# Performance work log

Hardware: AMD Instinct MI355X
Metric: run time of the kernel (lower is better)

Reference implementation:

```python
import jax, jax.numpy as jnp
import numpy as np

WEIGHT = 0.1

SOBEL_X = jnp.array([[-1.,0.,1.],[-2.,0.,2.],[-1.,0.,1.]], jnp.float32).reshape(1,1,3,3)
SOBEL_Y = jnp.array([[-1.,-2.,-1.],[0.,0.,0.],[1.,2.,1.]], jnp.float32).reshape(1,1,3,3)
LAPLACIAN = jnp.array([[0.,1.,0.],[1.,-4.,1.],[0.,1.,0.]], jnp.float32).reshape(1,1,3,3)


def _conv3x3(x, k):
    # x: [B,1,H,W], k: [1,1,3,3], SAME padding (pad=1)
    return jax.lax.conv_general_dilated(x, k, (1, 1), ((1, 1), (1, 1)),
                                         dimension_numbers=('NCHW', 'OIHW', 'NCHW'))


def _extract_dem_features(dem):
    gx = _conv3x3(dem, SOBEL_X)
    gy = _conv3x3(dem, SOBEL_Y)
    gmag = jnp.sqrt(gx * gx + gy * gy + 1e-8)
    gmag = (gmag - gmag.min()) / (gmag.max() - gmag.min() + 1e-8)  # global min/max like torch
    hnorm = (dem - dem.min()) / (dem.max() - dem.min() + 1e-8)
    curv = jnp.tanh(_conv3x3(dem, LAPLACIAN) * 0.1)
    return jnp.concatenate([gmag, hnorm, curv], axis=1)  # [B,3,H,W]


def _connectivity_one(mask):
    # mask: [H,W] float32 in {0,1}; 4-connected component labeling via min-label propagation
    H, W = mask.shape
    sentinel = H * W
    fg = mask > 0
    init = jnp.where(fg, jnp.arange(H * W, dtype=jnp.int32).reshape(H, W), sentinel)

    def body(state):
        lbl, _ = state
        pad = jnp.pad(lbl, 1, constant_values=sentinel)
        nb = jnp.minimum(jnp.minimum(pad[:-2, 1:-1], pad[2:, 1:-1]),
                         jnp.minimum(pad[1:-1, :-2], pad[1:-1, 2:]))
        new = jnp.where(fg, jnp.minimum(lbl, nb), sentinel)
        return new, jnp.any(new != lbl)

    lbl, _ = jax.lax.while_loop(lambda s: s[1], body, (init, jnp.array(True)))
    sizes = jax.ops.segment_sum(mask.reshape(-1), lbl.reshape(-1), num_segments=sentinel + 1)[:sentinel]
    total = mask.sum()
    ratio = sizes.max() / jnp.maximum(total, 1.0)
    # matches scipy path: 0 if no components; (1 - main_region_ratio) otherwise
    # (single component gives ratio==1 -> 0, same as scipy's len(sizes)>1 branch)
    return jnp.where(total > 0, 1.0 - ratio, 0.0)


def _connectivity_loss(pred_prob):
    mask = (pred_prob[:, 0] > 0.5).astype(jnp.float32)  # [B,H,W]
    per_sample = jax.vmap(_connectivity_one)(mask)
    return per_sample.sum() / pred_prob.shape[0]


def _scale_consistency_loss(pred_prob):
    B, _, H, W = pred_prob.shape
    area = pred_prob.sum(axis=(1, 2, 3))
    total_pixels = H * W
    tmin, tmax = 0.1 * total_pixels, 0.3 * total_pixels
    loss = jnp.mean(jax.nn.relu(area - tmax) + jax.nn.relu(tmin - area))
    return loss / total_pixels


def reference(pred_prob, dem):
    dem_features = _extract_dem_features(dem)              # [B,3,H,W]
    pred_features = jnp.broadcast_to(pred_prob, dem_features.shape)
    similarity = jnp.mean((pred_features - dem_features) ** 2)
    conn = _connectivity_loss(pred_prob)
    scale = _scale_consistency_loss(pred_prob)
    total = similarity + 0.1 * conn + 0.05 * scale
    return WEIGHT * total


def setup_inputs() -> dict:
    key = jax.random.key(0)
    k1, k2 = jax.random.split(key)
    B, H, W = 16, 512, 512
    pred_prob = jax.random.uniform(k1, (B, 1, H, W), dtype=jnp.float32)  # post-sigmoid probs
    dem = jax.random.normal(k2, (B, 1, H, W), dtype=jnp.float32)
    return {"pred_prob": pred_prob, "dem": dem}
```

## Files before the change

### kernel.cpp

```cpp
#include <hip/hip_runtime.h>
#include <math.h>

#define IMG_B 16
#define IMG_H 512
#define IMG_W 512
#define IMG_HW (IMG_H * IMG_W)
#define NPART 2048

#define NMOM 9

#define TILES 256
#define NODES_PER_TILE 192
#define NODES_PER_IMG (TILES * NODES_PER_TILE)
#define PAIRS 128
#define TOUCH (1 << 30)

struct Scal {
    float gmin, gmax, dmin, dmax;
    double mom[NMOM];
    double area[IMG_B];
    int fgcnt[IMG_B];
    int maxcnt[IMG_B];
};

#define OFF_PMM   512
#define OFF_MOM   33280
#define OFF_FG    180736
#define OFF_SCR   188928

__device__ __forceinline__ int uf_findv(const int* L, int p) {
    while (true) { const int q = ((volatile const int*)L)[p]; if (q == p) return p; p = q; }
}
__device__ __forceinline__ void uf_merge(int* L, int a, int b) {
    while (true) {
        a = uf_findv(L, a);
        b = uf_findv(L, b);
        if (a == b) return;
        if (a < b) { int t = a; a = b; b = t; }
        const int old = atomicMin(&L[a], b);
        if (old == a) return;
        a = old;
    }
}

__device__ __forceinline__ int run_start(unsigned m, int b) {
    const unsigned below = ~m & ((b == 0) ? 0u : ((1u << b) - 1u));
    return below ? (int)(32u - (unsigned)__builtin_clz(below)) : 0;
}
__device__ __forceinline__ int run_len(unsigned m, int s) {
    const unsigned inv = ~(m >> s);
    return inv ? __builtin_ctz(inv) : (32 - s);
}
__device__ __forceinline__ int run_idx(unsigned sm, int c) {
    return __popc(sm & (unsigned)((2ull << c) - 1ull)) - 1;
}
__device__ __forceinline__ unsigned spread4(unsigned x) {
    x &= 0xFFu;
    x = (x | (x << 12)) & 0x000F000Fu;
    x = (x | (x << 6))  & 0x03030303u;
    x = (x | (x << 3))  & 0x11111111u;
    return x;
}

__device__ __forceinline__ void ring_decode(int i, int& x, int& y) {
    if (i < 32)      { x = i;      y = 0;      }
    else if (i < 64) { x = i - 32; y = 31;     }
    else if (i < 94) { x = 0;      y = i - 63; }
    else             { x = 31;     y = i - 93; }
}

__global__ void k_main(const float* __restrict__ dem, const float* __restrict__ pred,
                       float4* __restrict__ pmm, double* __restrict__ pblk,
                       int* __restrict__ pfg,
                       int* __restrict__ Lp, int* __restrict__ Cp,
                       int* __restrict__ nslot, int* __restrict__ pairmax,
                       int b0, int nloc, int featOn) {
    __shared__ double smem_d[4104];
    int* smem = (int*)smem_d;
    const int tid = threadIdx.x;
    const int lane = tid & 63, wid = tid >> 6;

    if (blockIdx.x >= 32) {
        if (!featOn) return;
        const int fb = blockIdx.x - 32;
        const int b = blockIdx.y;
        const size_t off = (size_t)b * IMG_HW;
        const float* d = dem + off;
        const float* p = pred + off;
        const int base = fb * 2048 + tid * 8;
        const int y = base >> 9;

        const float4 z4 = make_float4(0.f, 0.f, 0.f, 0.f);
        float4 m0 = *(const float4*)(d + base);
        float4 m1 = *(const float4*)(d + base + 4);
        float4 u0 = z4, u1 = z4, w0 = z4, w1 = z4;
        if (y > 0)   { u0 = *(const float4*)(d + base - 512); u1 = *(const float4*)(d + base - 508); }
        if (y < 511) { w0 = *(const float4*)(d + base + 512); w1 = *(const float4*)(d + base + 516); }

        float uu[10], mm[10], ww[10];
        { float t;
          t = __shfl(m1.w, lane - 1); mm[0] = (lane > 0)  ? t : 0.f;
          t = __shfl(m0.x, lane + 1); mm[9] = (lane < 63) ? t : 0.f;
          t = __shfl(u1.w, lane - 1); uu[0] = (lane > 0)  ? t : 0.f;
          t = __shfl(u0.x, lane + 1); uu[9] = (lane < 63) ? t : 0.f;
          t = __shfl(w1.w, lane - 1); ww[0] = (lane > 0)  ? t : 0.f;
          t = __shfl(w0.x, lane + 1); ww[9] = (lane < 63) ? t : 0.f; }
        uu[1]=u0.x; uu[2]=u0.y; uu[3]=u0.z; uu[4]=u0.w; uu[5]=u1.x; uu[6]=u1.y; uu[7]=u1.z; uu[8]=u1.w;
        mm[1]=m0.x; mm[2]=m0.y; mm[3]=m0.z; mm[4]=m0.w; mm[5]=m1.x; mm[6]=m1.y; mm[7]=m1.z; mm[8]=m1.w;
        ww[1]=w0.x; ww[2]=w0.y; ww[3]=w0.z; ww[4]=w0.w; ww[5]=w1.x; ww[6]=w1.y; ww[7]=w1.z; ww[8]=w1.w;

        const float4 p0 = *(const float4*)(p + base);
        const float4 p1 = *(const float4*)(p + base + 4);
        const float pv[8] = {p0.x, p0.y, p0.z, p0.w, p1.x, p1.y, p1.z, p1.w};

        float gmn = 3.4e38f, gmx = -3.4e38f, dmn = 3.4e38f, dmx = -3.4e38f;
        float mf[NMOM];
#pragma unroll
        for (int m = 0; m < NMOM; ++m) mf[m] = 0.f;
        int fg = 0;
#pragma unroll
        for (int j = 0; j < 8; ++j) {
            const float gx = (uu[j+2] - uu[j]) + 2.f * (mm[j+2] - mm[j]) + (ww[j+2] - ww[j]);
            const float gy = (ww[j] - uu[j]) + 2.f * (ww[j+1] - uu[j+1]) + (ww[j+2] - uu[j+2]);
            const float gm = sqrtf(gx * gx + gy * gy + 1e-8f);
            const float lap = uu[j+1] + mm[j] + mm[j+2] + ww[j+1] - 4.f * mm[j+1];
            const float cv = tanhf(lap * 0.1f);
            const float pj = pv[j], dj = mm[j+1];
            gmn = fminf(gmn, gm); gmx = fmaxf(gmx, gm);
            dmn = fminf(dmn, dj); dmx = fmaxf(dmx, dj);
            fg += (pj > 0.5f) ? 1 : 0;
            const float et = pj - cv;
            mf[0] += pj;  mf[1] += pj * pj;
            mf[2] += gm;  mf[3] += gm * gm;  mf[4] += pj * gm;
            mf[5] += dj;  mf[6] += dj * dj;  mf[7] += pj * dj;
            mf[8] += et * et;
        }

        for (int o = 32; o > 0; o >>= 1) {
            gmn = fminf(gmn, __shfl_down(gmn, o));
            gmx = fmaxf(gmx, __shfl_down(gmx, o));
            dmn = fminf(dmn, __shfl_down(dmn, o));
            dmx = fmaxf(dmx, __shfl_down(dmx, o));
#pragma unroll
            for (int m = 0; m < NMOM; ++m) mf[m] += __shfl_down(mf[m], o);
            fg += __shfl_down(fg, o);
        }
        double (*sa)[NMOM] = (double(*)[NMOM])smem_d;
        float* sg0 = (float*)(smem_d + 36);
        float* sg1 = sg0 + 4; float* sd0 = sg0 + 8; float* sd1 = sg0 + 12;
        int* sf = (int*)(sg0 + 16);
        if (lane == 0) {
            sg0[wid] = gmn; sg1[wid] = gmx; sd0[wid] = dmn; sd1[wid] = dmx; sf[wid] = fg;
#pragma unroll
            for (int m = 0; m < NMOM; ++m) sa[wid][m] = (double)mf[m];
        }
        __syncthreads();
        if (tid == 0) {
            double mo[NMOM];
#pragma unroll
            for (int m = 0; m < NMOM; ++m) mo[m] = sa[0][m];
            for (int w = 1; w < 4; ++w) {
                gmn = fminf(gmn, sg0[w]); gmx = fmaxf(gmx, sg1[w]);
                dmn = fminf(dmn, sd0[w]); dmx = fmaxf(dmx, sd1[w]);
                fg += sf[w];
#pragma unroll
                for (int m = 0; m < NMOM; ++m) mo[m] += sa[w][m];
            }
            const int bid = b * 128 + fb;
            pmm[bid] = make_float4(gmn, gmx, dmn, dmx);
#pragma unroll
            for (int m = 0; m < NMOM; ++m) pblk[(size_t)bid * NMOM + m] = mo[m];
            pfg[bid] = fg;
        }
        return;
    }

    if (blockIdx.y >= nloc) return;
    const int slot = blockIdx.y;
    const float* p = pred + (size_t)(b0 + slot) * IMG_HW;
    int* L = Lp + (size_t)slot * NODES_PER_IMG;
    int* C = Cp + (size_t)slot * NODES_PER_IMG;
    const int pair = blockIdx.x * 4 + wid;
    const int tile0 = pair * 2;
    const int half = lane >> 5;
    const int tile = tile0 + half;
    const int tx0 = (tile0 & 15) * 32;
    const int ty  = (tile0 >> 4) * 32;
    const int r = lane & 31;

    int* lab  = smem;
    int* lcnt = smem + 4096;
    int* ns   = smem + 8192;
    int* labw = lab + wid * 1024;
    int* lcw  = lcnt + wid * 1024;
    int* nsw  = ns + wid * 2;
    if (lane < 2) nsw[lane] = 0;
    const int nbase = half * 512;

    const int myit = r >> 2;
    unsigned long long q0 = 0, q1 = 0, q2 = 0, q3 = 0;
    for (int it = 0; it < 8; ++it) {
        const int row = it * 4 + (lane >> 4);
        const float4 v = *(const float4*)(p + (ty + row) * IMG_W + tx0 + (lane & 15) * 4);
        const unsigned long long t0 = __ballot(v.x > 0.5f);
        const unsigned long long t1 = __ballot(v.y > 0.5f);
        const unsigned long long t2 = __ballot(v.z > 0.5f);
        const unsigned long long t3 = __ballot(v.w > 0.5f);
        if (it == myit) { q0 = t0; q1 = t1; q2 = t2; q3 = t3; }
    }
#pragma unroll
    for (int k = 0; k < 16; ++k) {
        const int n = k * 64 + lane;
        labw[n] = n; lcw[n] = 0;
    }
    const int sh = 16 * (r & 3) + 8 * half;
    const unsigned m = spread4((unsigned)(q0 >> sh))
                     | (spread4((unsigned)(q1 >> sh)) << 1)
                     | (spread4((unsigned)(q2 >> sh)) << 2)
                     | (spread4((unsigned)(q3 >> sh)) << 3);
    const int mpl = __shfl((int)m, lane - 1);
    const unsigned mp = (r >= 1) ? (unsigned)mpl : 0u;

    const unsigned sm  = m  & ~(m << 1);
    const unsigned smp = mp & ~(mp << 1);

    if (r >= 1) {
        unsigned ov = m & mp;
        while (ov) {
            const int bpos = __builtin_ctz(ov);
            const int sa2 = run_start(m, bpos);
            const int ea = sa2 + run_len(m, sa2) - 1;
            const int sb = run_start(mp, bpos);
            const int eb = sb + run_len(mp, sb) - 1;
            uf_merge(labw, nbase + run_idx(sm, sa2) * 32 + r,
                            nbase + run_idx(smp, sb) * 32 + (r - 1));
            const int e = (ea < eb) ? ea : eb;
            ov = (e >= 31) ? 0u : (ov & ~((1u << (e + 1)) - 1u));
        }
    }

    {
        unsigned rs = sm; int j = 0;
        while (rs) {
            const int st = __builtin_ctz(rs); rs &= rs - 1;
            const int len = run_len(m, st);
            const int e = st + len - 1;
            const int node = nbase + j * 32 + r; ++j;
            const int root = uf_findv(labw, node);
            if (root != node) labw[node] = root;
            atomicAdd(&lcw[root], len);
            if (r == 0 || r == 31 || st == 0 || e == 31)
                atomicOr(&lcw[root], TOUCH);
        }
    }

    int locmax = 0;
    {
        unsigned rs = sm; int j = 0;
        while (rs) {
            rs &= rs - 1;
            const int node = nbase + j * 32 + r; ++j;
            if (labw[node] != node) continue;
            const int c = lcw[node];
            if (c & TOUCH) {
                const int sl = atomicAdd(&nsw[half], 1);
                const int gn = tile * NODES_PER_TILE + 128 + sl;
                L[gn] = gn;
                C[gn] = c & ~TOUCH;
                lcw[node] = gn;
            } else {
                locmax = max(locmax, c);
            }
        }
    }
    for (int o = 32; o > 0; o >>= 1) locmax = max(locmax, __shfl_down(locmax, o));

#pragma unroll
    for (int t = 0; t < 4; ++t) {
        const int i = lane + t * 64;
        const int h = i >> 7, idx = i & 127;
        const int tb = (tile0 + h) * NODES_PER_TILE;
        if (idx < 124) {
            int x, yy;
            ring_decode(idx, x, yy);
            const unsigned my = (unsigned)__shfl((int)m, h * 32 + yy);
            int val = -1;
            if ((my >> x) & 1u) {
                const unsigned smy = my & ~(my << 1);
                const int node = h * 512 + run_idx(smy, x) * 32 + yy;
                const int root = uf_findv(labw, node);
                val = lcw[root];
            }
            L[tb + idx] = val;
        } else {
            L[tb + idx] = -1;
        }
    }

    if (lane == 0) pairmax[slot * PAIRS + pair] = locmax;
    if (lane < 2) nslot[slot * TILES + tile0 + lane] = nsw[lane];
}

__global__ void k_red(const float4* __restrict__ pmm, const double* __restrict__ pblk,
                      const int* __restrict__ pfg, Scal* s) {
    const int wid = threadIdx.x >> 6, lane = threadIdx.x & 63;
    if (blockIdx.x < IMG_B) {
        const int b = blockIdx.x;
        double ar = 0.0; int fg = 0;
        if (threadIdx.x < 128) {
            const int k = b * 128 + threadIdx.x;
            ar = pblk[(size_t)k * NMOM + 0];
            fg = pfg[k];
        }
        for (int o = 32; o > 0; o >>= 1) { ar += __shfl_down(ar, o); fg += __shfl_down(fg, o); }
        __shared__ double sa[4];
        __shared__ int sf[4];
        if (lane == 0) { sa[wid] = ar; sf[wid] = fg; }
        __syncthreads();
        if (threadIdx.x == 0) {
            ar += sa[1]; fg += sf[1];
            s->area[b] = ar; s->fgcnt[b] = fg;
            s->maxcnt[b] = 0;
        }
    } else if (blockIdx.x == IMG_B) {
        float gmn = 3.4e38f, gmx = -3.4e38f, dmn = 3.4e38f, dmx = -3.4e38f;
        for (int k = threadIdx.x; k < NPART; k += 256) {
            const float4 v = pmm[k];
            gmn = fminf(gmn, v.x); gmx = fmaxf(gmx, v.y);
            dmn = fminf(dmn, v.z); dmx = fmaxf(dmx, v.w);
        }
        for (int o = 32; o > 0; o >>= 1) {
            gmn = fminf(gmn, __shfl_down(gmn, o));
            gmx = fmaxf(gmx, __shfl_down(gmx, o));
            dmn = fminf(dmn, __shfl_down(dmn, o));
            dmx = fmaxf(dmx, __shfl_down(dmx, o));
        }
        __shared__ float sg0[4], sg1[4], sd0[4], sd1[4];
        if (lane == 0) { sg0[wid] = gmn; sg1[wid] = gmx; sd0[wid] = dmn; sd1[wid] = dmx; }
        __syncthreads();
        if (threadIdx.x == 0) {
            for (int w = 1; w < 4; ++w) {
                gmn = fminf(gmn, sg0[w]); gmx = fmaxf(gmx, sg1[w]);
                dmn = fminf(dmn, sd0[w]); dmx = fmaxf(dmx, sd1[w]);
            }
            s->gmin = gmn; s->gmax = gmx; s->dmin = dmn; s->dmax = dmx;
        }
    } else {
        const int m = blockIdx.x - IMG_B - 1;
        double acc = 0.0;
        for (int k = threadIdx.x; k < NPART; k += 256) acc += pblk[(size_t)k * NMOM + m];
        for (int o = 32; o > 0; o >>= 1) acc += __shfl_down(acc, o);
        __shared__ double sa[4];
        if (lane == 0) sa[wid] = acc;
        __syncthreads();
        if (threadIdx.x == 0) {
            for (int w = 1; w < 4; ++w) acc += sa[w];
            s->mom[m] = acc;
        }
    }
}

__global__ void k_bmerge(int* __restrict__ Lp) {
    const int slot = blockIdx.y;
    int* L = Lp + (size_t)slot * NODES_PER_IMG;
    const int e = blockIdx.x * 256 + threadIdx.x;
    int a, b;
    if (e < 7680) {
        const int sc = e / 512, y = e - sc * 512;
        const int ly = y & 31;
        const int tL = (y >> 5) * 16 + sc;
        const int iL = (ly == 0) ? 31 : (ly == 31) ? 63 : (93 + ly);
        const int iR = (ly == 0) ? 0  : (ly == 31) ? 32 : (63 + ly);
        a = tL * NODES_PER_TILE + iL;
        b = (tL + 1) * NODES_PER_TILE + iR;
    } else {
        const int e2 = e - 7680;
        const int sr = e2 / 512, x = e2 - sr * 512;
        const int lx = x & 31;
        const int tT = sr * 16 + (x >> 5);
        a = tT * NODES_PER_TILE + 32 + lx;
        b = (tT + 16) * NODES_PER_TILE + lx;
    }
    if (L[a] >= 0 && L[b] >= 0) uf_merge(L, a, b);
}

__global__ void k_lflush(const int* __restrict__ Lp, int* __restrict__ Cp,
                         const int* __restrict__ nslot) {
    const int img = blockIdx.y;
    const int* L = Lp + (size_t)img * NODES_PER_IMG;
    int* C = Cp + (size_t)img * NODES_PER_IMG;
    const int sidx = blockIdx.x * 256 + threadIdx.x;
    const int tile = sidx >> 6, sl = sidx & 63;
    if (sl >= nslot[img * TILES + tile]) return;
    const int g = tile * NODES_PER_TILE + 128 + sl;
    const int rt = uf_findv(L, g);
    if (rt != g) atomicAdd(&C[rt], C[g]);
}

__global__ void k_lmax(const int* __restrict__ Lp, const int* __restrict__ Cp,
                       const int* __restrict__ nslot, const int* __restrict__ pairmax,
                       Scal* s, int b0) {
    const int img = blockIdx.y;
    int m = 0;
    if (blockIdx.x < 64) {
        const int* L = Lp + (size_t)img * NODES_PER_IMG;
        const int* C = Cp + (size_t)img * NODES_PER_IMG;
        const int sidx = blockIdx.x * 256 + threadIdx.x;
        const int tile = sidx >> 6, sl = sidx & 63;
        if (sl < nslot[img * TILES + tile]) {
            const int g = tile * NODES_PER_TILE + 128 + sl;
            if (L[g] == g) m = C[g];
        }
    } else {
        if (threadIdx.x < PAIRS) m = pairmax[img * PAIRS + threadIdx.x];
    }
    for (int o = 32; o > 0; o >>= 1) m = max(m, __shfl_down(m, o));
    __shared__ int sm[4];
    const int wid = threadIdx.x >> 6, lane = threadIdx.x & 63;
    if (lane == 0) sm[wid] = m;
    __syncthreads();
    if (threadIdx.x == 0) {
        for (int w = 1; w < 4; ++w) m = max(m, sm[w]);
        if (m > 0) atomicMax(&s->maxcnt[b0 + img], m);
    }
}

__global__ void k_final(const Scal* __restrict__ s, float* __restrict__ out) {
    const double N = (double)IMG_B * (double)IMG_HW;
    const float gdenf = s->gmax - s->gmin + 1e-8f;
    const float ddenf = s->dmax - s->dmin + 1e-8f;
    const double a = 1.0 / (double)gdenf, bb = 1.0 / (double)ddenf;
    const double gmin = (double)s->gmin, dmin = (double)s->dmin;
    const double S_p = s->mom[0], S_pp = s->mom[1];
    const double S_g = s->mom[2], S_gg = s->mom[3], S_pg = s->mom[4];
    const double S_d = s->mom[5], S_dd = s->mom[6], S_pd = s->mom[7];
    const double S_t = s->mom[8];
    const double sum_g = S_pp - 2.0 * a * (S_pg - gmin * S_p)
                       + a * a * (S_gg - 2.0 * gmin * S_g + gmin * gmin * N);
    const double sum_d = S_pp - 2.0 * bb * (S_pd - dmin * S_p)
                       + bb * bb * (S_dd - 2.0 * dmin * S_d + dmin * dmin * N);
    const double sim = (sum_g + sum_d + S_t) / (3.0 * N);

    const double tp = (double)IMG_HW;
    const double tmin = 0.1 * tp, tmax = 0.3 * tp;
    double conn = 0.0, scale = 0.0;
    for (int b = 0; b < IMG_B; ++b) {
        const int total = s->fgcnt[b];
        if (total > 0) conn += 1.0 - (double)s->maxcnt[b] / (double)total;
        const double ar = s->area[b];
        scale += fmax(ar - tmax, 0.0) + fmax(tmin - ar, 0.0);
    }
    conn /= (double)IMG_B;
    scale = (scale / (double)IMG_B) / tp;
    const double total = sim + 0.1 * conn + 0.05 * scale;
    out[0] = (float)(0.1 * total);
}

extern "C" void kernel_launch(void* const* d_in, const int* in_sizes, int n_in,
                              void* d_out, int out_size, void* d_ws, size_t ws_size,
                              hipStream_t stream) {
    const float* pred = (const float*)d_in[0];
    const float* dem  = (const float*)d_in[1];
    float* out = (float*)d_out;

    char* ws = (char*)d_ws;
    Scal* s = (Scal*)ws;
    float4* pmm  = (float4*)(ws + OFF_PMM);
    double* pblk = (double*)(ws + OFF_MOM);
    int*    pfg  = (int*)(ws + OFF_FG);
    int* scratch = (int*)(ws + OFF_SCR);
    const size_t avail_ints = (ws_size > OFF_SCR) ? (ws_size - OFF_SCR) / 4 : 0;
    const size_t per_img = 2ull * NODES_PER_IMG + TILES + PAIRS;

    long long chunk = (long long)(avail_ints / per_img);
    if (chunk < 1) chunk = 1;
    if (chunk > IMG_B) chunk = IMG_B;

    for (int b0 = 0; b0 < IMG_B; b0 += (int)chunk) {
        const int n = (int)((b0 + chunk <= IMG_B) ? chunk : (IMG_B - b0));
        int* Lp      = scratch;
        int* Cp      = scratch + (size_t)chunk * NODES_PER_IMG;
        int* nslotp  = scratch + 2ull * chunk * NODES_PER_IMG;
        int* pairmax = nslotp + (size_t)chunk * TILES;
        const int featOn = (b0 == 0) ? 1 : 0;
        const int gx = featOn ? 160 : 32;
        const int gy = featOn ? IMG_B : n;
        hipLaunchKernelGGL(k_main, dim3(gx, gy), dim3(256), 0, stream,
                           dem, pred, pmm, pblk, pfg, Lp, Cp, nslotp, pairmax,
                           b0, n, featOn);
        if (b0 == 0)
            hipLaunchKernelGGL(k_red, dim3(IMG_B + 1 + NMOM), dim3(256), 0, stream,
                               pmm, pblk, pfg, s);
        hipLaunchKernelGGL(k_bmerge, dim3(60, n), dim3(256), 0, stream, Lp);
        hipLaunchKernelGGL(k_lflush, dim3(64, n), dim3(256), 0, stream, Lp, Cp, nslotp);
        hipLaunchKernelGGL(k_lmax,   dim3(65, n), dim3(256), 0, stream,
                           Lp, Cp, nslotp, pairmax, s, b0);
    }

    hipLaunchKernelGGL(k_final, dim3(1), dim3(1), 0, stream, s, out);
}
```

Baseline: 69.07 us.

## Halve k_main block size and fuse label flush with max into one tail kernel

Drops k_main to 128 threads per block with twice as many blocks, so feature blocks cover 1024 pixels and CCL blocks hold two tile pairs, and partial buffers, offsets and the k_red reduction are resized to match. It also merges k_lflush and k_lmax into a single k_tail kernel. Each non-root boundary slot adds its count to its root and uses the atomicAdd return value as a candidate maximum, removing one launch and its grid-wide barrier. The running atomic sums should still reach the final component size at the last add, but this relies on the per-slot counts being final before the atomics run.

```diff
diff --git a/kernel.cpp b/kernel.cpp
--- a/kernel.cpp
+++ b/kernel.cpp
@@ -5,7 +5,7 @@
 #define IMG_H 512
 #define IMG_W 512
 #define IMG_HW (IMG_H * IMG_W)
-#define NPART 2048
+#define NPART 4096
 
 #define NMOM 9
 
@@ -24,9 +24,9 @@
 };
 
 #define OFF_PMM   512
-#define OFF_MOM   33280
-#define OFF_FG    180736
-#define OFF_SCR   188928
+#define OFF_MOM   66048
+#define OFF_FG    360960
+#define OFF_SCR   377344
 
 __device__ __forceinline__ int uf_findv(const int* L, int p) {
     while (true) { const int q = ((volatile const int*)L)[p]; if (q == p) return p; p = q; }
@@ -75,19 +75,19 @@
                        int* __restrict__ Lp, int* __restrict__ Cp,
                        int* __restrict__ nslot, int* __restrict__ pairmax,
                        int b0, int nloc, int featOn) {
-    __shared__ double smem_d[4104];
+    __shared__ double smem_d[2052];
     int* smem = (int*)smem_d;
     const int tid = threadIdx.x;
     const int lane = tid & 63, wid = tid >> 6;
 
-    if (blockIdx.x >= 32) {
+    if (blockIdx.x >= 64) {
         if (!featOn) return;
-        const int fb = blockIdx.x - 32;
+        const int fb = blockIdx.x - 64;
         const int b = blockIdx.y;
         const size_t off = (size_t)b * IMG_HW;
         const float* d = dem + off;
         const float* p = pred + off;
-        const int base = fb * 2048 + tid * 8;
+        const int base = fb * 1024 + tid * 8;
         const int y = base >> 9;
 
         const float4 z4 = make_float4(0.f, 0.f, 0.f, 0.f);
@@ -146,9 +146,9 @@
             fg += __shfl_down(fg, o);
         }
         double (*sa)[NMOM] = (double(*)[NMOM])smem_d;
-        float* sg0 = (float*)(smem_d + 36);
-        float* sg1 = sg0 + 4; float* sd0 = sg0 + 8; float* sd1 = sg0 + 12;
-        int* sf = (int*)(sg0 + 16);
+        float* sg0 = (float*)(smem_d + 18);
+        float* sg1 = sg0 + 2; float* sd0 = sg0 + 4; float* sd1 = sg0 + 6;
+        int* sf = (int*)(sg0 + 8);
         if (lane == 0) {
             sg0[wid] = gmn; sg1[wid] = gmx; sd0[wid] = dmn; sd1[wid] = dmx; sf[wid] = fg;
 #pragma unroll
@@ -158,15 +158,11 @@
         if (tid == 0) {
             double mo[NMOM];
 #pragma unroll
-            for (int m = 0; m < NMOM; ++m) mo[m] = sa[0][m];
-            for (int w = 1; w < 4; ++w) {
-                gmn = fminf(gmn, sg0[w]); gmx = fmaxf(gmx, sg1[w]);
-                dmn = fminf(dmn, sd0[w]); dmx = fmaxf(dmx, sd1[w]);
-                fg += sf[w];
-#pragma unroll
-                for (int m = 0; m < NMOM; ++m) mo[m] += sa[w][m];
-            }
-            const int bid = b * 128 + fb;
+            for (int m = 0; m < NMOM; ++m) mo[m] = sa[0][m] + sa[1][m];
+            gmn = fminf(gmn, sg0[1]); gmx = fmaxf(gmx, sg1[1]);
+            dmn = fminf(dmn, sd0[1]); dmx = fmaxf(dmx, sd1[1]);
+            fg += sf[1];
+            const int bid = b * 256 + fb;
             pmm[bid] = make_float4(gmn, gmx, dmn, dmx);
 #pragma unroll
             for (int m = 0; m < NMOM; ++m) pblk[(size_t)bid * NMOM + m] = mo[m];
@@ -180,7 +176,7 @@
     const float* p = pred + (size_t)(b0 + slot) * IMG_HW;
     int* L = Lp + (size_t)slot * NODES_PER_IMG;
     int* C = Cp + (size_t)slot * NODES_PER_IMG;
-    const int pair = blockIdx.x * 4 + wid;
+    const int pair = blockIdx.x * 2 + wid;
     const int tile0 = pair * 2;
     const int half = lane >> 5;
     const int tile = tile0 + half;
@@ -189,8 +185,8 @@
     const int r = lane & 31;
 
     int* lab  = smem;
-    int* lcnt = smem + 4096;
-    int* ns   = smem + 8192;
+    int* lcnt = smem + 2048;
+    int* ns   = smem + 4096;
     int* labw = lab + wid * 1024;
     int* lcw  = lcnt + wid * 1024;
     int* nsw  = ns + wid * 2;
@@ -306,19 +302,16 @@
     const int wid = threadIdx.x >> 6, lane = threadIdx.x & 63;
     if (blockIdx.x < IMG_B) {
         const int b = blockIdx.x;
-        double ar = 0.0; int fg = 0;
-        if (threadIdx.x < 128) {
-            const int k = b * 128 + threadIdx.x;
-            ar = pblk[(size_t)k * NMOM + 0];
-            fg = pfg[k];
-        }
+        const int k = b * 256 + threadIdx.x;
+        double ar = pblk[(size_t)k * NMOM + 0];
+        int fg = pfg[k];
         for (int o = 32; o > 0; o >>= 1) { ar += __shfl_down(ar, o); fg += __shfl_down(fg, o); }
         __shared__ double sa[4];
         __shared__ int sf[4];
         if (lane == 0) { sa[wid] = ar; sf[wid] = fg; }
         __syncthreads();
         if (threadIdx.x == 0) {
-            ar += sa[1]; fg += sf[1];
+            for (int w = 1; w < 4; ++w) { ar += sa[w]; fg += sf[w]; }
             s->area[b] = ar; s->fgcnt[b] = fg;
             s->maxcnt[b] = 0;
         }
@@ -384,32 +377,22 @@
     if (L[a] >= 0 && L[b] >= 0) uf_merge(L, a, b);
 }
 
-__global__ void k_lflush(const int* __restrict__ Lp, int* __restrict__ Cp,
-                         const int* __restrict__ nslot) {
-    const int img = blockIdx.y;
-    const int* L = Lp + (size_t)img * NODES_PER_IMG;
-    int* C = Cp + (size_t)img * NODES_PER_IMG;
-    const int sidx = blockIdx.x * 256 + threadIdx.x;
-    const int tile = sidx >> 6, sl = sidx & 63;
-    if (sl >= nslot[img * TILES + tile]) return;
-    const int g = tile * NODES_PER_TILE + 128 + sl;
-    const int rt = uf_findv(L, g);
-    if (rt != g) atomicAdd(&C[rt], C[g]);
-}
-
-__global__ void k_lmax(const int* __restrict__ Lp, const int* __restrict__ Cp,
+__global__ void k_tail(const int* __restrict__ Lp, int* __restrict__ Cp,
                        const int* __restrict__ nslot, const int* __restrict__ pairmax,
                        Scal* s, int b0) {
     const int img = blockIdx.y;
     int m = 0;
     if (blockIdx.x < 64) {
         const int* L = Lp + (size_t)img * NODES_PER_IMG;
-        const int* C = Cp + (size_t)img * NODES_PER_IMG;
+        int* C = Cp + (size_t)img * NODES_PER_IMG;
         const int sidx = blockIdx.x * 256 + threadIdx.x;
         const int tile = sidx >> 6, sl = sidx & 63;
         if (sl < nslot[img * TILES + tile]) {
             const int g = tile * NODES_PER_TILE + 128 + sl;
-            if (L[g] == g) m = C[g];
+            const int sz = C[g];
+            const int rt = uf_findv(L, g);
+            if (rt != g) m = atomicAdd(&C[rt], sz) + sz;
+            else         m = sz;
         }
     } else {
         if (threadIdx.x < PAIRS) m = pairmax[img * PAIRS + threadIdx.x];
@@ -483,17 +466,16 @@
         int* nslotp  = scratch + 2ull * chunk * NODES_PER_IMG;
         int* pairmax = nslotp + (size_t)chunk * TILES;
         const int featOn = (b0 == 0) ? 1 : 0;
-        const int gx = featOn ? 160 : 32;
+        const int gx = featOn ? 320 : 64;
         const int gy = featOn ? IMG_B : n;
-        hipLaunchKernelGGL(k_main, dim3(gx, gy), dim3(256), 0, stream,
+        hipLaunchKernelGGL(k_main, dim3(gx, gy), dim3(128), 0, stream,
                            dem, pred, pmm, pblk, pfg, Lp, Cp, nslotp, pairmax,
                            b0, n, featOn);
         if (b0 == 0)
             hipLaunchKernelGGL(k_red, dim3(IMG_B + 1 + NMOM), dim3(256), 0, stream,
                                pmm, pblk, pfg, s);
         hipLaunchKernelGGL(k_bmerge, dim3(60, n), dim3(256), 0, stream, Lp);
-        hipLaunchKernelGGL(k_lflush, dim3(64, n), dim3(256), 0, stream, Lp, Cp, nslotp);
-        hipLaunchKernelGGL(k_lmax,   dim3(65, n), dim3(256), 0, stream,
+        hipLaunchKernelGGL(k_tail,   dim3(65, n), dim3(256), 0, stream,
                            Lp, Cp, nslotp, pairmax, s, b0);
     }
 
```

Result: no change. 68.12 us (-1.4%).
